# Performance work log

Hardware: AMD Instinct MI355X
Metric: run time of the kernel (lower is better)

## Reference

```python
import jax, jax.numpy as jnp
import numpy as np

N = 100000   # nodes
E = 1600000  # edges
D = 128      # out_feats
V = 5000     # annotation_size
L = 3        # n_steps SAGE layers


def setup_inputs() -> dict:
    key = jax.random.key(0)
    k0, k1, k2, k3, k4 = jax.random.split(key, 5)
    annotation = jax.random.randint(k0, (N,), 0, V)
    src = jax.random.randint(k1, (E,), 0, N)
    dst = jax.random.randint(k2, (E,), 0, N)
    emb = jax.random.normal(k3, (V, D), dtype=jnp.float32) * 0.02
    Ws = jax.random.normal(k4, (L, D, D), dtype=jnp.float32) / np.sqrt(D).astype(np.float32)
    bs = jnp.zeros((L, D), dtype=jnp.float32)
    return {"annotation": annotation, "src": src, "dst": dst, "emb": emb, "Ws": Ws, "bs": bs}


def reference(annotation, src, dst, emb, Ws, bs):
    # tok_embedding == 2: embedding lookup of node token ids
    h = emb[annotation]                                              # [N, D]
    # in-degree per destination node (constant across layers)
    deg = jax.ops.segment_sum(jnp.ones_like(src, dtype=jnp.float32), dst, num_segments=N)
    inv = 1.0 / (deg + 1.0)                                          # [N]
    # DGL SAGEConv, aggregator_type='gcn', eval mode (feat_drop is identity):
    #   h_neigh = (h_self + sum_{u->v} h_u) / (in_deg + 1); rst = relu(h_neigh @ W + b)
    for l in range(L):
        agg = jax.ops.segment_sum(h[src], dst, num_segments=N)       # [N, D] gather-scatter
        h = jax.nn.relu(((h + agg) * inv[:, None]) @ Ws[l] + bs[l])
    # residual=False -> merged node features are just h ('_merge_on nodes h')
    return h
```

## Files before the change

### kernel.cpp

```cpp
#include <hip/hip_runtime.h>
#include <hip/hip_fp16.h>


#define D 128

typedef float f32x4 __attribute__((ext_vector_type(4)));
typedef _Float16 f16x8 __attribute__((ext_vector_type(8)));

__global__ void k_count(const int* __restrict__ dst, int* __restrict__ deg, int E) {
    int e = blockIdx.x * blockDim.x + threadIdx.x;
    if (e < E) atomicAdd(&deg[dst[e]], 1);
}

__global__ void k_bsum(const int* __restrict__ deg, int* __restrict__ bsum, int n) {
    __shared__ int s[256];
    int t = threadIdx.x, i = blockIdx.x * 256 + t;
    s[t] = (i < n) ? deg[i] : 0;
    __syncthreads();
    for (int off = 128; off > 0; off >>= 1) { if (t < off) s[t] += s[t + off]; __syncthreads(); }
    if (t == 0) bsum[blockIdx.x] = s[0];
}

__global__ void k_scanb(int* __restrict__ bsum, int nb, int* __restrict__ row_ptr, int N, int E) {
    __shared__ int s[512];
    int t = threadIdx.x;
    int v = (t < nb) ? bsum[t] : 0;
    s[t] = v;
    __syncthreads();
    for (int off = 1; off < 512; off <<= 1) {
        int x = (t >= off) ? s[t - off] : 0;
        __syncthreads();
        s[t] += x;
        __syncthreads();
    }
    if (t < nb) bsum[t] = s[t] - v;
    if (t == 0) row_ptr[N] = E;
}

__global__ void k_scan_local(int* __restrict__ deg, const int* __restrict__ bpre,
                             int* __restrict__ row_ptr, int n) {
    __shared__ int s[256];
    int t = threadIdx.x, i = blockIdx.x * 256 + t;
    int v = (i < n) ? deg[i] : 0;
    s[t] = v;
    __syncthreads();
    for (int off = 1; off < 256; off <<= 1) {
        int x = (t >= off) ? s[t - off] : 0;
        __syncthreads();
        s[t] += x;
        __syncthreads();
    }
    if (i < n) {
        row_ptr[i] = bpre[blockIdx.x] + s[t] - v;
        deg[i] = 0;
    }
}

__global__ void k_fill(const int* __restrict__ src, const int* __restrict__ dst,
                       const int* __restrict__ ann, const int* __restrict__ row_ptr,
                       int* __restrict__ cur, int2* __restrict__ eal, int E) {
    int e = blockIdx.x * blockDim.x + threadIdx.x;
    if (e >= E) return;
    int d = dst[e];
    int s = src[e];
    int pos = atomicAdd(&cur[d], 1);
    eal[row_ptr[d] + pos] = make_int2(s, ann[s]);
}

union H16Chunk { float4 f4; __half2 h2[4]; __half h[8]; };

__global__ void k_h16(const float* __restrict__ x, __half* __restrict__ y, int n8) {
    int i = blockIdx.x * blockDim.x + threadIdx.x;
    if (i >= n8) return;
    const float4* p = (const float4*)x;
    float4 a = p[2 * i], b = p[2 * i + 1];
    H16Chunk u;
    u.h2[0] = __floats2half2_rn(a.x, a.y);
    u.h2[1] = __floats2half2_rn(a.z, a.w);
    u.h2[2] = __floats2half2_rn(b.x, b.y);
    u.h2[3] = __floats2half2_rn(b.z, b.w);
    *(float4*)&y[8 * i] = u.f4;
}

#define XT_LD 136
__global__ __launch_bounds__(256) void k_gemm_mfma(
    const __half* __restrict__ x16, const float* __restrict__ W,
    __half* __restrict__ g16, int n, int ntiles) {
    __shared__ __half Bf[8 * 4 * 64 * 8];
    __shared__ __half Xt[64 * XT_LD];
    int tid = threadIdx.x;
    int lane = tid & 63;
    int wv = tid >> 6;

    for (int idx = tid; idx < 8 * 4 * 64; idx += 256) {
        int l = idx & 63, ks = (idx >> 6) & 3, nt = idx >> 8;
        int kq = (l >> 4) * 8;
        int col = nt * 16 + (l & 15);
        H16Chunk u;
        #pragma unroll
        for (int j = 0; j < 8; j++)
            u.h[j] = __float2half(W[(ks * 32 + kq + j) * 128 + col]);
        *(float4*)&Bf[idx * 8] = u.f4;
    }
    __syncthreads();

    f16x8 breg[8][4];
    #pragma unroll
    for (int nt = 0; nt < 8; nt++)
        #pragma unroll
        for (int ks = 0; ks < 4; ks++)
            breg[nt][ks] = *(f16x8*)&Bf[((nt * 4 + ks) * 64 + lane) * 8];

    int srow = tid >> 2;
    int sc = (tid & 3) * 32;
    int m = lane & 15, quad = lane >> 4;

    for (int tile = blockIdx.x; tile < ntiles; tile += gridDim.x) {
        int row0 = tile * 64;
        __syncthreads();
        {
            int gr = row0 + srow;
            if (gr >= n) gr = n - 1;
            const float4* xp = (const float4*)&x16[(size_t)gr * 128 + sc];
            float4 v0 = xp[0], v1 = xp[1], v2 = xp[2], v3 = xp[3];
            float4* xd = (float4*)&Xt[srow * XT_LD + sc];
            xd[0] = v0; xd[1] = v1; xd[2] = v2; xd[3] = v3;
        }
        __syncthreads();

        f32x4 acc[8];
        #pragma unroll
        for (int nt = 0; nt < 8; nt++) acc[nt] = (f32x4){0.f, 0.f, 0.f, 0.f};
        #pragma unroll
        for (int ks = 0; ks < 4; ks++) {
            f16x8 a = *(f16x8*)&Xt[(wv * 16 + m) * XT_LD + ks * 32 + quad * 8];
            #pragma unroll
            for (int nt = 0; nt < 8; nt++)
                acc[nt] = __builtin_amdgcn_mfma_f32_16x16x32_f16(a, breg[nt][ks], acc[nt], 0, 0, 0);
        }
        __syncthreads();
        #pragma unroll
        for (int nt = 0; nt < 8; nt++)
            #pragma unroll
            for (int r = 0; r < 4; r++)
                Xt[(wv * 16 + quad * 4 + r) * XT_LD + nt * 16 + m] = __float2half(acc[nt][r]);
        __syncthreads();
        {
            int gr = row0 + srow;
            if (gr < n) {
                float4* gp = (float4*)&g16[(size_t)gr * 128 + sc];
                float4* xs = (float4*)&Xt[srow * XT_LD + sc];
                gp[0] = xs[0]; gp[1] = xs[1]; gp[2] = xs[2]; gp[3] = xs[3];
            }
        }
    }
}

template<bool SELY, bool OUT32>
__global__ __launch_bounds__(256) void k_agg(
    const float4* __restrict__ tab, const int* __restrict__ selfidx,
    const int* __restrict__ row_ptr, const int2* __restrict__ eal,
    const float4* __restrict__ bias4,
    __half* __restrict__ h16out, float* __restrict__ f32out, int n) {
    int v = blockIdx.x * 4 + (threadIdx.x >> 6);
    int lane = threadIdx.x & 63;
    int g = lane >> 4;
    int q = lane & 15;
    int beg = row_ptr[v], end = row_ptr[v + 1];
    int deg = end - beg;
    float acc[8] = {};

    #define ACCUM(raw) do { H16Chunk u; u.f4 = (raw);                          \
        float2 t0 = __half22float2(u.h2[0]); acc[0] += t0.x; acc[1] += t0.y;   \
        float2 t1 = __half22float2(u.h2[1]); acc[2] += t1.x; acc[3] += t1.y;   \
        float2 t2 = __half22float2(u.h2[2]); acc[4] += t2.x; acc[5] += t2.y;   \
        float2 t3 = __half22float2(u.h2[3]); acc[6] += t3.x; acc[7] += t3.y; } while (0)
    #define IDX(w) (SELY ? (w).y : (w).x)

    if (g == 0) {
        int sr = SELY ? selfidx[v] : v;
        ACCUM(tab[(size_t)sr * 16 + q]);
    }

    int quads = deg >> 2;
    int p = 0;
    for (; p + 4 <= quads; p += 4) {
        int eb = beg + 4 * p + g;
        int2 w0 = eal[eb + 0], w1 = eal[eb + 4], w2 = eal[eb + 8], w3 = eal[eb + 12];
        float4 r0 = tab[(size_t)IDX(w0) * 16 + q], r1 = tab[(size_t)IDX(w1) * 16 + q];
        float4 r2 = tab[(size_t)IDX(w2) * 16 + q], r3 = tab[(size_t)IDX(w3) * 16 + q];
        ACCUM(r0); ACCUM(r1); ACCUM(r2); ACCUM(r3);
    }
    for (; p < quads; p++) ACCUM(tab[(size_t)IDX(eal[beg + 4 * p + g]) * 16 + q]);
    int tail = deg & 3;
    if (g < tail) ACCUM(tab[(size_t)IDX(eal[beg + 4 * quads + g]) * 16 + q]);
    #undef ACCUM
    #undef IDX

    #pragma unroll
    for (int j = 0; j < 8; j++) {
        acc[j] += __shfl_down(acc[j], 16, 64);
        acc[j] += __shfl_down(acc[j], 32, 64);
    }
    if (g == 0) {
        float sc = 1.0f / (float)(deg + 1);
        float4 b0 = bias4[2 * q], b1 = bias4[2 * q + 1];
        float o[8];
        o[0] = fmaxf(acc[0] * sc + b0.x, 0.f);
        o[1] = fmaxf(acc[1] * sc + b0.y, 0.f);
        o[2] = fmaxf(acc[2] * sc + b0.z, 0.f);
        o[3] = fmaxf(acc[3] * sc + b0.w, 0.f);
        o[4] = fmaxf(acc[4] * sc + b1.x, 0.f);
        o[5] = fmaxf(acc[5] * sc + b1.y, 0.f);
        o[6] = fmaxf(acc[6] * sc + b1.z, 0.f);
        o[7] = fmaxf(acc[7] * sc + b1.w, 0.f);
        if (!OUT32) {
            H16Chunk u;
            u.h2[0] = __floats2half2_rn(o[0], o[1]);
            u.h2[1] = __floats2half2_rn(o[2], o[3]);
            u.h2[2] = __floats2half2_rn(o[4], o[5]);
            u.h2[3] = __floats2half2_rn(o[6], o[7]);
            *(float4*)&h16out[(size_t)v * 128 + q * 8] = u.f4;
        } else {
            f32x4 a = {o[0], o[1], o[2], o[3]};
            f32x4 b = {o[4], o[5], o[6], o[7]};
            __builtin_nontemporal_store(a, (f32x4*)&f32out[(size_t)v * 128 + q * 8]);
            __builtin_nontemporal_store(b, (f32x4*)&f32out[(size_t)v * 128 + q * 8 + 4]);
        }
    }
}

extern "C" void kernel_launch(void* const* d_in, const int* in_sizes, int n_in,
                              void* d_out, int out_size, void* d_ws, size_t ws_size,
                              hipStream_t stream) {
    const int*   ann = (const int*)d_in[0];
    const int*   src = (const int*)d_in[1];
    const int*   dst = (const int*)d_in[2];
    const float* emb = (const float*)d_in[3];
    const float* Ws  = (const float*)d_in[4];
    const float* bs  = (const float*)d_in[5];
    float* out = (float*)d_out;

    const int N = in_sizes[0];
    const int E = in_sizes[1];
    const int V = in_sizes[3] / D;
    const int NB   = (N + 255) / 256;
    const int NT64 = (N + 63) / 64;
    const int VT64 = (V + 63) / 64;

    int*  deg     = (int*)d_ws;
    int*  row_ptr = deg + N;
    int*  bsum    = row_ptr + ((N + 1 + 3) & ~3);
    int2* eal     = (int2*)(bsum + 512);
    __half* hA16  = (__half*)(eal + E);
    __half* gB16  = hA16 + (size_t)N * D;
    __half* embW16= gB16 + (size_t)N * D;
    __half* emb16 = embW16 + (size_t)V * D;

    k_h16<<<(V * D / 8 + 255) / 256, 256, 0, stream>>>(emb, emb16, V * D / 8);
    k_gemm_mfma<<<VT64, 256, 0, stream>>>(emb16, Ws, embW16, V, VT64);

    hipMemsetAsync(deg, 0, (size_t)N * sizeof(int), stream);
    k_count<<<(E + 255) / 256, 256, 0, stream>>>(dst, deg, E);
    k_bsum<<<NB, 256, 0, stream>>>(deg, bsum, N);
    k_scanb<<<1, 512, 0, stream>>>(bsum, NB, row_ptr, N, E);
    k_scan_local<<<NB, 256, 0, stream>>>(deg, bsum, row_ptr, N);
    k_fill<<<(E + 255) / 256, 256, 0, stream>>>(src, dst, ann, row_ptr, deg, eal, E);

    k_agg<true, false><<<N / 4, 256, 0, stream>>>(
        (const float4*)embW16, ann, row_ptr, eal, (const float4*)bs,
        hA16, nullptr, N);

    k_gemm_mfma<<<512, 256, 0, stream>>>(hA16, Ws + (size_t)D * D, gB16, N, NT64);
    k_agg<false, false><<<N / 4, 256, 0, stream>>>(
        (const float4*)gB16, nullptr, row_ptr, eal, (const float4*)(bs + D),
        hA16, nullptr, N);

    k_gemm_mfma<<<512, 256, 0, stream>>>(hA16, Ws + (size_t)2 * D * D, gB16, N, NT64);
    k_agg<false, true><<<N / 4, 256, 0, stream>>>(
        (const float4*)gB16, nullptr, row_ptr, eal, (const float4*)(bs + 2 * D),
        nullptr, out, N);
}
```

Measured before the change: 481.3 us.

## Build CSR with two-pass bucketed counting sort using shared-memory atomics

```diff
diff --git a/kernel.cpp b/kernel.cpp
--- a/kernel.cpp
+++ b/kernel.cpp
@@ -3,68 +3,108 @@
 
 
 #define D 128
+#define PBLK 128
+#define BSH 7
 
 typedef float f32x4 __attribute__((ext_vector_type(4)));
 typedef _Float16 f16x8 __attribute__((ext_vector_type(8)));
 
-__global__ void k_count(const int* __restrict__ dst, int* __restrict__ deg, int E) {
-    int e = blockIdx.x * blockDim.x + threadIdx.x;
-    if (e < E) atomicAdd(&deg[dst[e]], 1);
-}
-
-__global__ void k_bsum(const int* __restrict__ deg, int* __restrict__ bsum, int n) {
-    __shared__ int s[256];
-    int t = threadIdx.x, i = blockIdx.x * 256 + t;
-    s[t] = (i < n) ? deg[i] : 0;
-    __syncthreads();
-    for (int off = 128; off > 0; off >>= 1) { if (t < off) s[t] += s[t + off]; __syncthreads(); }
-    if (t == 0) bsum[blockIdx.x] = s[0];
-}
-
-__global__ void k_scanb(int* __restrict__ bsum, int nb, int* __restrict__ row_ptr, int N, int E) {
-    __shared__ int s[512];
+__global__ __launch_bounds__(256) void k_hist(
+    const int* __restrict__ dst, int* __restrict__ hist,
+    int E, int chunk, int nbk) {
+    __shared__ int lh[1024];
+    int j = blockIdx.x, tid = threadIdx.x;
+    for (int i = tid; i < nbk; i += 256) lh[i] = 0;
+    __syncthreads();
+    int e0 = j * chunk, e1 = min(E, e0 + chunk);
+    for (int e = e0 + tid; e < e1; e += 256)
+        atomicAdd(&lh[dst[e] >> BSH], 1);
+    __syncthreads();
+    for (int i = tid; i < nbk; i += 256) hist[(size_t)j * nbk + i] = lh[i];
+}
+
+__global__ void k_scan_offs(int* __restrict__ hist, int* __restrict__ tot, int nbk) {
+    __shared__ int s[PBLK];
+    int b = blockIdx.x, j = threadIdx.x;
+    int v = hist[(size_t)j * nbk + b];
+    s[j] = v;
+    __syncthreads();
+    for (int off = 1; off < PBLK; off <<= 1) {
+        int x = (j >= off) ? s[j - off] : 0;
+        __syncthreads();
+        s[j] += x;
+        __syncthreads();
+    }
+    hist[(size_t)j * nbk + b] = s[j] - v;
+    if (j == PBLK - 1) tot[b] = s[j];
+}
+
+__global__ void k_scan_tot(int* __restrict__ tot, int* __restrict__ row_ptr,
+                           int nbk, int N, int E) {
+    __shared__ int s[1024];
     int t = threadIdx.x;
-    int v = (t < nb) ? bsum[t] : 0;
+    int v = (t < nbk) ? tot[t] : 0;
     s[t] = v;
     __syncthreads();
-    for (int off = 1; off < 512; off <<= 1) {
+    for (int off = 1; off < 1024; off <<= 1) {
         int x = (t >= off) ? s[t - off] : 0;
         __syncthreads();
         s[t] += x;
         __syncthreads();
     }
-    if (t < nb) bsum[t] = s[t] - v;
-    if (t == 0) row_ptr[N] = E;
-}
-
-__global__ void k_scan_local(int* __restrict__ deg, const int* __restrict__ bpre,
-                             int* __restrict__ row_ptr, int n) {
-    __shared__ int s[256];
-    int t = threadIdx.x, i = blockIdx.x * 256 + t;
-    int v = (i < n) ? deg[i] : 0;
-    s[t] = v;
-    __syncthreads();
-    for (int off = 1; off < 256; off <<= 1) {
-        int x = (t >= off) ? s[t - off] : 0;
-        __syncthreads();
-        s[t] += x;
-        __syncthreads();
-    }
-    if (i < n) {
-        row_ptr[i] = bpre[blockIdx.x] + s[t] - v;
-        deg[i] = 0;
-    }
-}
-
-__global__ void k_fill(const int* __restrict__ src, const int* __restrict__ dst,
-                       const int* __restrict__ ann, const int* __restrict__ row_ptr,
-                       int* __restrict__ cur, int2* __restrict__ eal, int E) {
-    int e = blockIdx.x * blockDim.x + threadIdx.x;
-    if (e >= E) return;
-    int d = dst[e];
-    int s = src[e];
-    int pos = atomicAdd(&cur[d], 1);
-    eal[row_ptr[d] + pos] = make_int2(s, ann[s]);
+    if (t < nbk) tot[t] = s[t] - v;
+    if (t == 0) { tot[nbk] = E; row_ptr[N] = E; }
+}
+
+__global__ __launch_bounds__(256) void k_scatter(
+    const int* __restrict__ src, const int* __restrict__ dst,
+    const int* __restrict__ ann, const int* __restrict__ hist,
+    const int* __restrict__ tot, int2* __restrict__ tmp,
+    int E, int chunk, int nbk) {
+    __shared__ int cur[1024];
+    int j = blockIdx.x, tid = threadIdx.x;
+    for (int i = tid; i < nbk; i += 256)
+        cur[i] = tot[i] + hist[(size_t)j * nbk + i];
+    __syncthreads();
+    int e0 = j * chunk, e1 = min(E, e0 + chunk);
+    for (int e = e0 + tid; e < e1; e += 256) {
+        int d = dst[e], s = src[e];
+        int p = atomicAdd(&cur[d >> BSH], 1);
+        tmp[p] = make_int2(s, ((d & ((1 << BSH) - 1)) << 13) | ann[s]);
+    }
+}
+
+__global__ __launch_bounds__(256) void k_place(
+    const int2* __restrict__ tmp, const int* __restrict__ tot,
+    int* __restrict__ row_ptr, int2* __restrict__ eal, int N) {
+    __shared__ int cnt[1 << BSH], sc[1 << BSH];
+    int b = blockIdx.x, tid = threadIdx.x;
+    int base = tot[b], end = tot[b + 1];
+    if (tid < (1 << BSH)) cnt[tid] = 0;
+    __syncthreads();
+    for (int i = base + tid; i < end; i += 256)
+        atomicAdd(&cnt[((unsigned)tmp[i].y) >> 13], 1);
+    __syncthreads();
+    if (tid < (1 << BSH)) sc[tid] = cnt[tid];
+    __syncthreads();
+    for (int off = 1; off < (1 << BSH); off <<= 1) {
+        int x = (tid < (1 << BSH) && tid >= off) ? sc[tid - off] : 0;
+        __syncthreads();
+        if (tid < (1 << BSH)) sc[tid] += x;
+        __syncthreads();
+    }
+    if (tid < (1 << BSH)) {
+        int excl = sc[tid] - cnt[tid];
+        int d0 = (b << BSH) + tid;
+        if (d0 < N) row_ptr[d0] = base + excl;
+        cnt[tid] = excl;
+    }
+    __syncthreads();
+    for (int i = base + tid; i < end; i += 256) {
+        int2 w = tmp[i];
+        int p = atomicAdd(&cnt[((unsigned)w.y) >> 13], 1);
+        eal[base + p] = make_int2(w.x, w.y & 0x1FFF);
+    }
 }
 
 union H16Chunk { float4 f4; __half2 h2[4]; __half h[8]; };
@@ -244,9 +284,10 @@
     const int N = in_sizes[0];
     const int E = in_sizes[1];
     const int V = in_sizes[3] / D;
-    const int NB   = (N + 255) / 256;
     const int NT64 = (N + 63) / 64;
     const int VT64 = (V + 63) / 64;
+    const int NBK  = (N + (1 << BSH) - 1) >> BSH;
+    const int CHK  = (E + PBLK - 1) / PBLK;
 
     int*  deg     = (int*)d_ws;
     int*  row_ptr = deg + N;
@@ -256,16 +297,18 @@
     __half* gB16  = hA16 + (size_t)N * D;
     __half* embW16= gB16 + (size_t)N * D;
     __half* emb16 = embW16 + (size_t)V * D;
+    int2* tmp  = (int2*)hA16;
+    int*  hist = (int*)gB16;
+    int*  tot  = hist + (size_t)PBLK * NBK;
 
     k_h16<<<(V * D / 8 + 255) / 256, 256, 0, stream>>>(emb, emb16, V * D / 8);
     k_gemm_mfma<<<VT64, 256, 0, stream>>>(emb16, Ws, embW16, V, VT64);
 
-    hipMemsetAsync(deg, 0, (size_t)N * sizeof(int), stream);
-    k_count<<<(E + 255) / 256, 256, 0, stream>>>(dst, deg, E);
-    k_bsum<<<NB, 256, 0, stream>>>(deg, bsum, N);
-    k_scanb<<<1, 512, 0, stream>>>(bsum, NB, row_ptr, N, E);
-    k_scan_local<<<NB, 256, 0, stream>>>(deg, bsum, row_ptr, N);
-    k_fill<<<(E + 255) / 256, 256, 0, stream>>>(src, dst, ann, row_ptr, deg, eal, E);
+    k_hist<<<PBLK, 256, 0, stream>>>(dst, hist, E, CHK, NBK);
+    k_scan_offs<<<NBK, PBLK, 0, stream>>>(hist, tot, NBK);
+    k_scan_tot<<<1, 1024, 0, stream>>>(tot, row_ptr, NBK, N, E);
+    k_scatter<<<PBLK, 256, 0, stream>>>(src, dst, ann, hist, tot, tmp, E, CHK, NBK);
+    k_place<<<NBK, 256, 0, stream>>>(tmp, tot, row_ptr, eal, N);
 
     k_agg<true, false><<<N / 4, 256, 0, stream>>>(
         (const float4*)embW16, ann, row_ptr, eal, (const float4*)bs,
```

Result: faster. 417.5 us (-13.3%).
